# Kernel optimization log

Measured on AMD Instinct MI355X. Metric: run time of the kernel, lower is better.

Reference implementation:

```python
import jax, jax.numpy as jnp
import numpy as np

DIM = 1024
N_HEADS = 16
HEAD_DIM = DIM // N_HEADS
FF_DIM = 4096
EPS = 1e-8


def rms_norm(x, scale):
    # norm = ||x||_2 * d^{-1/2}; out = scale * x / (norm + eps)
    norm = jnp.linalg.norm(x, axis=-1, keepdims=True) * (x.shape[-1] ** -0.5)
    return scale * x / (norm + EPS)


def rope_cos_sin(seq_len, dtype=jnp.float32):
    # inv_freq over even indices of head_dim; after the truncation branch in
    # apply_rotary_pos_emb, effective cos/sin have size head_dim//2.
    inv_freq = 1.0 / (10000.0 ** (jnp.arange(0, HEAD_DIM, 2, dtype=jnp.float32) / HEAD_DIM))
    t = jnp.arange(seq_len, dtype=jnp.float32)
    freqs = t[:, None] * inv_freq[None, :]  # [S, head_dim//2]
    return jnp.cos(freqs).astype(dtype), jnp.sin(freqs).astype(dtype)


def apply_rope(x, cos, sin):
    # x: [B, S, H, hd]; cos/sin: [S, hd//2] broadcast over batch and heads
    c = cos[None, :, None, :]
    s = sin[None, :, None, :]
    x1, x2 = jnp.split(x, 2, axis=-1)
    return jnp.concatenate([x1 * c - x2 * s, x1 * s + x2 * c], axis=-1)


def setup_inputs() -> dict:
    key = jax.random.key(0)
    ks = jax.random.split(key, 10)
    B, S = 2, 2048
    std = DIM ** -0.5
    inp = {
        "x": jax.random.normal(ks[0], (B, S, DIM), jnp.float32),
        "mask": jnp.tril(jnp.ones((S, S), dtype=bool)),
        "qkv_w": jax.random.normal(ks[1], (3 * DIM, DIM), jnp.float32) * std,
        "attn_out_w": jax.random.normal(ks[2], (DIM, DIM), jnp.float32) * std,
        "gate_w": jax.random.normal(ks[3], (FF_DIM, DIM), jnp.float32) * std,
        "gate_b": jnp.zeros((FF_DIM,), jnp.float32),
        "lin_w": jax.random.normal(ks[4], (FF_DIM, DIM), jnp.float32) * std,
        "lin_b": jnp.zeros((FF_DIM,), jnp.float32),
        "ff_out_w": jax.random.normal(ks[5], (DIM, FF_DIM), jnp.float32) * (FF_DIM ** -0.5),
        "norm1_scale": jnp.ones((DIM,), jnp.float32),
        "norm2_scale": jnp.ones((DIM,), jnp.float32),
    }
    return inp


def reference(x, mask, qkv_w, attn_out_w, gate_w, gate_b, lin_w, lin_b,
              ff_out_w, norm1_scale, norm2_scale):
    B, S, _ = x.shape
    residual = x
    qkv = (x @ qkv_w.T).reshape(B, S, 3, N_HEADS, HEAD_DIM)
    q, k, v = qkv[:, :, 0], qkv[:, :, 1], qkv[:, :, 2]  # [B,S,H,hd]
    cos, sin = rope_cos_sin(S, x.dtype)
    q = apply_rope(q, cos, sin)
    k = apply_rope(k, cos, sin)
    # naive full attention, materializing [B,H,S,S] as the source does
    scores = jnp.einsum('bqhd,bkhd->bhqk', q, k) / jnp.sqrt(jnp.asarray(HEAD_DIM, x.dtype))
    scores = jnp.where(mask[None, None, :, :], scores, jnp.asarray(-1e9, x.dtype))
    attn = jax.nn.softmax(scores, axis=-1)
    out = jnp.einsum('bhqk,bkhd->bqhd', attn, v).reshape(B, S, DIM)
    out = out @ attn_out_w.T
    x = rms_norm(residual + out, norm1_scale)
    residual = x
    ff = jax.nn.sigmoid(x @ gate_w.T + gate_b) * (x @ lin_w.T + lin_b)
    ff = ff @ ff_out_w.T
    x = rms_norm(residual + ff, norm2_scale)
    return x
```

## Files before the change

kernel.cpp:

```cpp
#include <hip/hip_runtime.h>
#include <hip/hip_bf16.h>
#include <math.h>

#define DIMSZ 1024
#define NHEAD 16
#define HDIM 64
#define FFDIM 4096
#define SEQ 2048
#define NBATCH 2

typedef unsigned short ushortt;
typedef __attribute__((ext_vector_type(8))) short frag8;
typedef __attribute__((ext_vector_type(4))) float f32x4;

__device__ __forceinline__ float u2f(ushortt u) {
  return __uint_as_float(((unsigned)u) << 16);
}
__device__ __forceinline__ ushortt f2bu(float f) {
  unsigned x = __float_as_uint(f);
  return (ushortt)((x + 0x7FFFu + ((x >> 16) & 1u)) >> 16);
}

__global__ __launch_bounds__(256) void cast_f2b(
    const float* __restrict__ src, ushortt* __restrict__ dst, int n) {
  int i = (blockIdx.x * 256 + threadIdx.x) * 4;
  if (i >= n) return;
  float4 f = *(const float4*)(src + i);
  ushort4 u;
  u.x = f2bu(f.x); u.y = f2bu(f.y); u.z = f2bu(f.z); u.w = f2bu(f.w);
  *(ushort4*)(dst + i) = u;
}

__global__ __launch_bounds__(256) void zero_f32(float* __restrict__ p, int n) {
  int i = (blockIdx.x * 256 + threadIdx.x) * 4;
  if (i < n) *(float4*)(p + i) = make_float4(0.f, 0.f, 0.f, 0.f);
}

template <int EPI, int SK>
__global__ __launch_bounds__(256) void gemm_mfma(
    const ushortt* __restrict__ A, const ushortt* __restrict__ W,
    void* __restrict__ Cv, int M, int N, int K, int KB, size_t skoff) {
  __shared__ __align__(16) short As[2][128 * 32];
  __shared__ __align__(16) short Bs[2][128 * 32];
  const int tid = threadIdx.x;
  const int wave = tid >> 6;
  const int lane = tid & 63;
  int xcd = blockIdx.x & 7, r = blockIdx.x >> 3, kz = 0;
  if (SK == 2) { kz = r & 1; r >>= 1; }
  const int bm = (xcd * 4 + (r & 3)) * 128;
  const int bn = (r >> 2) * 128;
  const int ko0 = kz * KB;
  const int wm = (wave >> 1) * 64;
  const int wn = (wave & 1) * 64;

  f32x4 acc[4][4] = {};

  const int sr = lane >> 2;
  const int sc = (lane & 3) * 8;
  const ushortt* pa0 = A + (size_t)(bm + wave * 16 + sr) * K + ko0 + sc;
  const ushortt* pa1 = pa0 + (size_t)64 * K;
  const ushortt* pb0 = W + (size_t)(bn + wave * 16 + sr) * K + ko0 + sc;
  const ushortt* pb1 = pb0 + (size_t)64 * K;
  const int lo0 = (wave * 16) * 32;
  const int lo1 = (64 + wave * 16) * 32;

  const int fr = lane & 15;
  const int fq = (lane >> 4) * 8;
  const int nt = KB >> 5;

  auto stage = [&](int t, int buf) {
    const int ko = t * 32;
    short* ab = &As[0][0] + buf * 4096;
    short* bb = &Bs[0][0] + buf * 4096;
    __builtin_amdgcn_global_load_lds(
        (const __attribute__((address_space(1))) void*)(pa0 + ko),
        (__attribute__((address_space(3))) void*)(ab + lo0), 16, 0, 0);
    __builtin_amdgcn_global_load_lds(
        (const __attribute__((address_space(1))) void*)(pa1 + ko),
        (__attribute__((address_space(3))) void*)(ab + lo1), 16, 0, 0);
    __builtin_amdgcn_global_load_lds(
        (const __attribute__((address_space(1))) void*)(pb0 + ko),
        (__attribute__((address_space(3))) void*)(bb + lo0), 16, 0, 0);
    __builtin_amdgcn_global_load_lds(
        (const __attribute__((address_space(1))) void*)(pb1 + ko),
        (__attribute__((address_space(3))) void*)(bb + lo1), 16, 0, 0);
  };

  stage(0, 0);
  __syncthreads();

  for (int t = 0; t < nt; ++t) {
    if (t + 1 < nt) stage(t + 1, (t + 1) & 1);
    const short* as = &As[0][0] + (t & 1) * 4096;
    const short* bs = &Bs[0][0] + (t & 1) * 4096;

    frag8 af[4], bf[4];
#pragma unroll
    for (int mi = 0; mi < 4; ++mi)
      af[mi] = *(const frag8*)&as[(wm + mi * 16 + fr) * 32 + fq];
#pragma unroll
    for (int ni = 0; ni < 4; ++ni)
      bf[ni] = *(const frag8*)&bs[(wn + ni * 16 + fr) * 32 + fq];
#pragma unroll
    for (int mi = 0; mi < 4; ++mi)
#pragma unroll
      for (int ni = 0; ni < 4; ++ni)
        acc[mi][ni] = __builtin_amdgcn_mfma_f32_16x16x32_bf16(
            af[mi], bf[ni], acc[mi][ni], 0, 0, 0);
    __syncthreads();
  }

  const int er = (lane >> 4) * 4;
  const int ec = lane & 15;
  float* C0 = (float*)Cv + (SK == 2 ? (size_t)kz * skoff : 0);
#pragma unroll
  for (int mi = 0; mi < 4; ++mi)
#pragma unroll
    for (int ni = 0; ni < 4; ++ni)
#pragma unroll
      for (int r2 = 0; r2 < 4; ++r2) {
        int m = bm + wm + mi * 16 + er + r2;
        int n = bn + wn + ni * 16 + ec;
        size_t o = (size_t)m * N + n;
        float v = acc[mi][ni][r2];
        if (EPI == 0) {
          C0[o] = v;
        } else {
          ((ushortt*)Cv)[o] = f2bu(v);
        }
      }
}

__global__ __launch_bounds__(256) void gemm_gatelin(
    const ushortt* __restrict__ A, const ushortt* __restrict__ Wg,
    const ushortt* __restrict__ Wl, ushortt* __restrict__ Cv,
    const float* __restrict__ gbias, const float* __restrict__ lbias,
    int M, int N, int K) {
  __shared__ __align__(16) short As[2][128 * 32];
  __shared__ __align__(16) short Gs[2][128 * 32];
  __shared__ __align__(16) short Ls[2][128 * 32];
  const int tid = threadIdx.x;
  const int wave = tid >> 6;
  const int lane = tid & 63;
  int xcd = blockIdx.x & 7, r = blockIdx.x >> 3;
  const int bm = (xcd * 4 + (r & 3)) * 128;
  const int bn = (r >> 2) * 128;
  const int wm = (wave >> 1) * 64;
  const int wn = (wave & 1) * 64;

  f32x4 accg[4][4] = {};
  f32x4 accl[4][4] = {};

  const int sr = lane >> 2;
  const int sc = (lane & 3) * 8;
  const ushortt* pa0 = A + (size_t)(bm + wave * 16 + sr) * K + sc;
  const ushortt* pa1 = pa0 + (size_t)64 * K;
  const ushortt* pg0 = Wg + (size_t)(bn + wave * 16 + sr) * K + sc;
  const ushortt* pg1 = pg0 + (size_t)64 * K;
  const ushortt* pl0 = Wl + (size_t)(bn + wave * 16 + sr) * K + sc;
  const ushortt* pl1 = pl0 + (size_t)64 * K;
  const int lo0 = (wave * 16) * 32;
  const int lo1 = (64 + wave * 16) * 32;

  const int fr = lane & 15;
  const int fq = (lane >> 4) * 8;
  const int nt = K >> 5;

  auto stage = [&](int t, int buf) {
    const int ko = t * 32;
    short* ab = &As[0][0] + buf * 4096;
    short* gb = &Gs[0][0] + buf * 4096;
    short* lb = &Ls[0][0] + buf * 4096;
    __builtin_amdgcn_global_load_lds(
        (const __attribute__((address_space(1))) void*)(pa0 + ko),
        (__attribute__((address_space(3))) void*)(ab + lo0), 16, 0, 0);
    __builtin_amdgcn_global_load_lds(
        (const __attribute__((address_space(1))) void*)(pa1 + ko),
        (__attribute__((address_space(3))) void*)(ab + lo1), 16, 0, 0);
    __builtin_amdgcn_global_load_lds(
        (const __attribute__((address_space(1))) void*)(pg0 + ko),
        (__attribute__((address_space(3))) void*)(gb + lo0), 16, 0, 0);
    __builtin_amdgcn_global_load_lds(
        (const __attribute__((address_space(1))) void*)(pg1 + ko),
        (__attribute__((address_space(3))) void*)(gb + lo1), 16, 0, 0);
    __builtin_amdgcn_global_load_lds(
        (const __attribute__((address_space(1))) void*)(pl0 + ko),
        (__attribute__((address_space(3))) void*)(lb + lo0), 16, 0, 0);
    __builtin_amdgcn_global_load_lds(
        (const __attribute__((address_space(1))) void*)(pl1 + ko),
        (__attribute__((address_space(3))) void*)(lb + lo1), 16, 0, 0);
  };

  stage(0, 0);
  __syncthreads();

  for (int t = 0; t < nt; ++t) {
    if (t + 1 < nt) stage(t + 1, (t + 1) & 1);
    const short* as = &As[0][0] + (t & 1) * 4096;
    const short* gs = &Gs[0][0] + (t & 1) * 4096;
    const short* ls = &Ls[0][0] + (t & 1) * 4096;

    frag8 af[4], gf[4], lf[4];
#pragma unroll
    for (int mi = 0; mi < 4; ++mi)
      af[mi] = *(const frag8*)&as[(wm + mi * 16 + fr) * 32 + fq];
#pragma unroll
    for (int ni = 0; ni < 4; ++ni) {
      gf[ni] = *(const frag8*)&gs[(wn + ni * 16 + fr) * 32 + fq];
      lf[ni] = *(const frag8*)&ls[(wn + ni * 16 + fr) * 32 + fq];
    }
#pragma unroll
    for (int mi = 0; mi < 4; ++mi)
#pragma unroll
      for (int ni = 0; ni < 4; ++ni) {
        accg[mi][ni] = __builtin_amdgcn_mfma_f32_16x16x32_bf16(
            af[mi], gf[ni], accg[mi][ni], 0, 0, 0);
        accl[mi][ni] = __builtin_amdgcn_mfma_f32_16x16x32_bf16(
            af[mi], lf[ni], accl[mi][ni], 0, 0, 0);
      }
    __syncthreads();
  }

  const int er = (lane >> 4) * 4;
  const int ec = lane & 15;
#pragma unroll
  for (int mi = 0; mi < 4; ++mi)
#pragma unroll
    for (int ni = 0; ni < 4; ++ni)
#pragma unroll
      for (int r2 = 0; r2 < 4; ++r2) {
        int m = bm + wm + mi * 16 + er + r2;
        int n = bn + wn + ni * 16 + ec;
        size_t o = (size_t)m * N + n;
        float g = accg[mi][ni][r2] + gbias[n];
        float l = accl[mi][ni][r2] + lbias[n];
        float sig = 1.0f / (1.0f + __expf(-g));
        ((ushortt*)Cv)[o] = f2bu(sig * l);
      }
}

__global__ __launch_bounds__(256) void gemm_ffout(
    const ushortt* __restrict__ A, const float* __restrict__ Bw,
    float* __restrict__ C, int koff) {
  __shared__ __align__(16) short As[2][128 * 32];
  __shared__ __align__(16) short Bs[2][128 * 32];
  const int tid = threadIdx.x;
  const int wave = tid >> 6;
  const int lane = tid & 63;
  int xcd = blockIdx.x & 7, r = blockIdx.x >> 3;
  const int kz = r & 1; r >>= 1;
  const int bm = (xcd * 4 + (r & 3)) * 128;
  const int bn = (r >> 2) * 128;
  const int wm = (wave >> 1) * 64;
  const int wn = (wave & 1) * 64;

  f32x4 acc[4][4] = {};

  const int sr = lane >> 2;
  const int sc = (lane & 3) * 8;
  const ushortt* pa0 = A + (size_t)(bm + wave * 16 + sr) * 2048 + kz * 1024 + sc;
  const ushortt* pa1 = pa0 + (size_t)64 * 2048;
  const int lo0 = (wave * 16) * 32;
  const int lo1 = (64 + wave * 16) * 32;

  const int br = tid >> 2;
  const int kc = (tid & 3) * 8;
  const float* pb0 = Bw + (size_t)(bn + br) * FFDIM + koff + kz * 1024 + kc;
  const float* pb1 = pb0 + (size_t)64 * FFDIM;

  const int fr = lane & 15;
  const int fq = (lane >> 4) * 8;
  const int nt = 1024 >> 5;

  float4 f0, f1, f2, f3;
  auto bload = [&](int t) {
    const float* p0 = pb0 + t * 32;
    const float* p1 = pb1 + t * 32;
    f0 = *(const float4*)p0; f1 = *(const float4*)(p0 + 4);
    f2 = *(const float4*)p1; f3 = *(const float4*)(p1 + 4);
  };
  auto pk = [&](float4 a, float4 b) {
    frag8 v;
    v[0] = (short)f2bu(a.x); v[1] = (short)f2bu(a.y);
    v[2] = (short)f2bu(a.z); v[3] = (short)f2bu(a.w);
    v[4] = (short)f2bu(b.x); v[5] = (short)f2bu(b.y);
    v[6] = (short)f2bu(b.z); v[7] = (short)f2bu(b.w);
    return v;
  };
  auto bwrite = [&](int buf) {
    *(frag8*)&Bs[buf][tid * 8] = pk(f0, f1);
    *(frag8*)&Bs[buf][2048 + tid * 8] = pk(f2, f3);
  };
  auto astage = [&](int t, int buf) {
    const int ko = t * 32;
    short* ab = &As[0][0] + buf * 4096;
    __builtin_amdgcn_global_load_lds(
        (const __attribute__((address_space(1))) void*)(pa0 + ko),
        (__attribute__((address_space(3))) void*)(ab + lo0), 16, 0, 0);
    __builtin_amdgcn_global_load_lds(
        (const __attribute__((address_space(1))) void*)(pa1 + ko),
        (__attribute__((address_space(3))) void*)(ab + lo1), 16, 0, 0);
  };

  astage(0, 0);
  bload(0);
  bwrite(0);
  __syncthreads();

  for (int t = 0; t < nt; ++t) {
    if (t + 1 < nt) {
      astage(t + 1, (t + 1) & 1);
      bload(t + 1);
    }
    const short* as = &As[0][0] + (t & 1) * 4096;
    const short* bs = &Bs[0][0] + (t & 1) * 4096;

    frag8 af[4], bf[4];
#pragma unroll
    for (int mi = 0; mi < 4; ++mi)
      af[mi] = *(const frag8*)&as[(wm + mi * 16 + fr) * 32 + fq];
#pragma unroll
    for (int ni = 0; ni < 4; ++ni)
      bf[ni] = *(const frag8*)&bs[(wn + ni * 16 + fr) * 32 + fq];
#pragma unroll
    for (int mi = 0; mi < 4; ++mi)
#pragma unroll
      for (int ni = 0; ni < 4; ++ni)
        acc[mi][ni] = __builtin_amdgcn_mfma_f32_16x16x32_bf16(
            af[mi], bf[ni], acc[mi][ni], 0, 0, 0);
    if (t + 1 < nt) bwrite((t + 1) & 1);
    __syncthreads();
  }

  const int er = (lane >> 4) * 4;
  const int ec = lane & 15;
#pragma unroll
  for (int mi = 0; mi < 4; ++mi)
#pragma unroll
    for (int ni = 0; ni < 4; ++ni)
#pragma unroll
      for (int r2 = 0; r2 < 4; ++r2) {
        int m = bm + wm + mi * 16 + er + r2;
        int n = bn + wn + ni * 16 + ec;
        unsafeAtomicAdd(C + (size_t)m * 1024 + n, acc[mi][ni][r2]);
      }
}

__global__ __launch_bounds__(256) void rope_prep(
    const ushortt* __restrict__ qkv, ushortt* __restrict__ Qr,
    ushortt* __restrict__ Kr, ushortt* __restrict__ Vr) {
  const int s0 = blockIdx.x * 64;
  const int bh = blockIdx.y;
  const int b = bh >> 4, h = bh & 15;
  const int tid = threadIdx.x;
  __shared__ float ifr_s[32];
  __shared__ ushortt vt[64][72];
  if (tid < 32) ifr_s[tid] = __powf(10000.0f, -(float)tid * (1.0f / 32.0f));
  __syncthreads();
  const size_t qbase = (size_t)bh * SEQ * 64;

#pragma unroll
  for (int i = 0; i < 8; ++i) {
    int p = i * 256 + tid;
    int r = p >> 5, d = p & 31;
    size_t src = ((size_t)(b * SEQ + s0 + r)) * (3 * DIMSZ) + h * 64 + d;
    float q1 = u2f(qkv[src]), q2 = u2f(qkv[src + 32]);
    float k1 = u2f(qkv[src + DIMSZ]), k2 = u2f(qkv[src + DIMSZ + 32]);
    float ang = (float)(s0 + r) * ifr_s[d];
    float sn, cs;
    __sincosf(ang, &sn, &cs);
    size_t dst = qbase + (size_t)(s0 + r) * 64 + d;
    Qr[dst]      = f2bu((q1 * cs - q2 * sn) * 0.125f);
    Qr[dst + 32] = f2bu((q1 * sn + q2 * cs) * 0.125f);
    Kr[dst]      = f2bu(k1 * cs - k2 * sn);
    Kr[dst + 32] = f2bu(k1 * sn + k2 * cs);
  }

#pragma unroll
  for (int i = 0; i < 2; ++i) {
    int e = (i * 256 + tid) * 8;
    int r = e >> 6, d0 = e & 63;
    size_t src = ((size_t)(b * SEQ + s0 + r)) * (3 * DIMSZ) + 2 * DIMSZ + h * 64 + d0;
    *(ushort4*)&vt[r][d0]     = *(const ushort4*)(qkv + src);
    *(ushort4*)&vt[r][d0 + 4] = *(const ushort4*)(qkv + src + 4);
  }
  __syncthreads();
  {
    int d = tid >> 2;
    int sc0 = (tid & 3) * 16;
    size_t dst = (size_t)bh * 64 * SEQ + (size_t)blockIdx.x * 4096 +
                 (size_t)d * 64 + sc0;
    ushortt tmp[16];
#pragma unroll
    for (int j = 0; j < 16; ++j) tmp[j] = vt[sc0 + j][d];
    *(ushort4*)(Vr + dst)      = *(ushort4*)&tmp[0];
    *(ushort4*)(Vr + dst + 4)  = *(ushort4*)&tmp[4];
    *(ushort4*)(Vr + dst + 8)  = *(ushort4*)&tmp[8];
    *(ushort4*)(Vr + dst + 12) = *(ushort4*)&tmp[12];
  }
}

__global__ __launch_bounds__(512) void flash_mfma(
    const ushortt* __restrict__ Qr, const ushortt* __restrict__ Kr,
    const ushortt* __restrict__ Vr, ushortt* __restrict__ ctx) {
  const int id = blockIdx.x;
  const int r5 = id & 255;
  const int qt0 = r5 >> 5;
  const int qt = (id & 256) ? (15 - qt0) : qt0;
  const int bh = r5 & 31;
  const int q0 = qt * 128;
  const int b = bh >> 4, h = bh & 15;
  const int tid = threadIdx.x;
  const int w = tid >> 6;
  const int lane = tid & 63;
  const int fr = lane & 15;
  const int quad = lane >> 4;

  __shared__ __align__(16) short Kb[2][4096];
  __shared__ __align__(16) short Vb[2][4096];
  __shared__ __align__(16) ushortt Ps[8][16][72];

  const size_t qkbase = (size_t)bh * SEQ * 64;
  const size_t vbase = (size_t)bh * 64 * SEQ;

  const int lin = (w << 10) + ((lane & 63) << 4);
  const int swz = lin ^ (((lin >> 7) & 7) << 4);
  const char* ksrc = (const char*)(Kr + qkbase) + swz;
  const char* vsrc = (const char*)(Vr + vbase) + swz;
  short* kdst[2] = {&Kb[0][w * 512], &Kb[1][w * 512]};
  short* vdst[2] = {&Vb[0][w * 512], &Vb[1][w * 512]};

  frag8 aq[2];
#pragma unroll
  for (int hh = 0; hh < 2; ++hh)
    aq[hh] = *(const frag8*)(Qr + qkbase + (size_t)(q0 + w * 16 + fr) * 64 +
                             hh * 32 + quad * 8);

  float mr[4], lr[4];
  f32x4 od[4] = {};
#pragma unroll
  for (int r = 0; r < 4; ++r) { mr[r] = -1e30f; lr[r] = 0.0f; }

  const int nt = 2 * qt + 2;

  __builtin_amdgcn_global_load_lds(
      (const __attribute__((address_space(1))) void*)ksrc,
      (__attribute__((address_space(3))) void*)kdst[0], 16, 0, 0);
  __builtin_amdgcn_global_load_lds(
      (const __attribute__((address_space(1))) void*)vsrc,
      (__attribute__((address_space(3))) void*)vdst[0], 16, 0, 0);
  __syncthreads();

  for (int t = 0; t < nt; ++t) {
    const int c0 = t * 64;
    if (t + 1 < nt) {
      const char* kn = ksrc + (size_t)(t + 1) * 8192;
      const char* vn = vsrc + (size_t)(t + 1) * 8192;
      __builtin_amdgcn_global_load_lds(
          (const __attribute__((address_space(1))) void*)kn,
          (__attribute__((address_space(3))) void*)kdst[(t + 1) & 1], 16, 0, 0);
      __builtin_amdgcn_global_load_lds(
          (const __attribute__((address_space(1))) void*)vn,
          (__attribute__((address_space(3))) void*)vdst[(t + 1) & 1], 16, 0, 0);
    }
    const char* kcur = (const char*)Kb[t & 1];
    const char* vcur = (const char*)Vb[t & 1];

    if (c0 <= q0 + w * 16 + 15) {
      f32x4 sc[4] = {};
#pragma unroll
      for (int ni = 0; ni < 4; ++ni)
#pragma unroll
        for (int hh = 0; hh < 2; ++hh) {
          int kb = (((ni * 16 + fr) << 7) + (hh << 6) + (quad << 4)) ^
                   ((fr & 7) << 4);
          frag8 kf = *(const frag8*)(kcur + kb);
          sc[ni] = __builtin_amdgcn_mfma_f32_16x16x32_bf16(aq[hh], kf, sc[ni],
                                                           0, 0, 0);
        }

      if (c0 + 63 > q0 + w * 16) {
        int rowb = q0 + w * 16 + quad * 4;
#pragma unroll
        for (int ni = 0; ni < 4; ++ni) {
          int col = c0 + ni * 16 + fr;
#pragma unroll
          for (int r = 0; r < 4; ++r)
            if (col > rowb + r) sc[ni][r] = -1e30f;
        }
      }

#pragma unroll
      for (int r = 0; r < 4; ++r) {
        float cm = fmaxf(fmaxf(sc[0][r], sc[1][r]), fmaxf(sc[2][r], sc[3][r]));
        for (int off = 1; off < 16; off <<= 1)
          cm = fmaxf(cm, __shfl_xor(cm, off, 16));
        float mn = fmaxf(mr[r], cm);
        float corr = __expf(mr[r] - mn);
        mr[r] = mn;
        float ps = 0.0f;
#pragma unroll
        for (int ni = 0; ni < 4; ++ni) {
          float p = __expf(sc[ni][r] - mn);
          Ps[w][quad * 4 + r][ni * 16 + fr] = f2bu(p);
          ps += p;
        }
        for (int off = 1; off < 16; off <<= 1) ps += __shfl_xor(ps, off, 16);
        lr[r] = lr[r] * corr + ps;
#pragma unroll
        for (int dt = 0; dt < 4; ++dt) od[dt][r] *= corr;
      }

      frag8 pf[2];
#pragma unroll
      for (int hh = 0; hh < 2; ++hh)
        pf[hh] = *(const frag8*)&Ps[w][fr][hh * 32 + quad * 8];
#pragma unroll
      for (int dt = 0; dt < 4; ++dt)
#pragma unroll
        for (int hh = 0; hh < 2; ++hh) {
          int vb_ = (((dt * 16 + fr) << 7) + (hh << 6) + (quad << 4)) ^
                    ((fr & 7) << 4);
          frag8 vf = *(const frag8*)(vcur + vb_);
          od[dt] = __builtin_amdgcn_mfma_f32_16x16x32_bf16(pf[hh], vf, od[dt],
                                                           0, 0, 0);
        }
    }
    __syncthreads();
  }

#pragma unroll
  for (int r = 0; r < 4; ++r) {
    float inv = 1.0f / lr[r];
    size_t row = (size_t)(b * SEQ + q0 + w * 16 + quad * 4 + r) * DIMSZ + h * 64;
#pragma unroll
    for (int dt = 0; dt < 4; ++dt)
      ctx[row + dt * 16 + fr] = f2bu(od[dt][r] * inv);
  }
}

template <int DUAL, int NP>
__global__ __launch_bounds__(256) void add_rmsnorm(
    const float* __restrict__ res, const float* __restrict__ pa,
    const float* __restrict__ pb, const float* __restrict__ scale,
    float* __restrict__ out, ushortt* __restrict__ out2) {
  const int row = blockIdx.x;
  const int tid = threadIdx.x;
  const size_t base = (size_t)row * DIMSZ;
  __shared__ float red[4];
  float y[4];
  float ss = 0.0f;
#pragma unroll
  for (int j = 0; j < 4; ++j) {
    int d = tid + j * 256;
    float yv = res[base + d] + pa[base + d];
    if (NP == 3) yv += pb[base + d];
    y[j] = yv;
    ss += yv * yv;
  }
  for (int off = 1; off < 64; off <<= 1) ss += __shfl_xor(ss, off, 64);
  if ((tid & 63) == 0) red[tid >> 6] = ss;
  __syncthreads();
  float tot = red[0] + red[1] + red[2] + red[3];
  float norm = sqrtf(tot) * 0.03125f;
  float inv = 1.0f / (norm + 1e-8f);
#pragma unroll
  for (int j = 0; j < 4; ++j) {
    int d = tid + j * 256;
    float v = scale[d] * y[j] * inv;
    out[base + d] = v;
    if (DUAL) out2[base + d] = f2bu(v);
  }
}

extern "C" void kernel_launch(void* const* d_in, const int* in_sizes, int n_in,
                              void* d_out, int out_size, void* d_ws, size_t ws_size,
                              hipStream_t stream) {
  const float* x          = (const float*)d_in[0];
  const float* qkv_w      = (const float*)d_in[2];
  const float* attn_out_w = (const float*)d_in[3];
  const float* gate_w     = (const float*)d_in[4];
  const float* gate_b     = (const float*)d_in[5];
  const float* lin_w      = (const float*)d_in[6];
  const float* lin_b      = (const float*)d_in[7];
  const float* ff_out_w   = (const float*)d_in[8];
  const float* n1s        = (const float*)d_in[9];
  const float* n2s        = (const float*)d_in[10];
  float* out = (float*)d_out;

  const int M = NBATCH * SEQ;
  char* ws = (char*)d_ws;
  char* dob = (char*)d_out;
  const size_t MB = 1 << 20;
  ushortt* qkv_tmp = (ushortt*)(ws + 0);
  ushortt* xb      = (ushortt*)(ws + 24 * MB);
  ushortt* qkv_wb  = (ushortt*)(ws + 32 * MB);
  ushortt* Qr      = (ushortt*)(ws + 24 * MB);
  ushortt* Kr      = (ushortt*)(ws + 32 * MB);
  ushortt* Vr      = (ushortt*)(ws + 40 * MB);
  ushortt* attn_wb = (ushortt*)(ws + 24 * MB);
  float*   proj_a  = (float*)(ws + 0);
  float*   proj_b  = (float*)(ws + 40 * MB);
  float*   x1      = (float*)(ws + 16 * MB);
  ushortt* x1b     = (ushortt*)(ws + 32 * MB);
  float*   proj2   = (float*)(ws + 0);
  ushortt* gcb     = (ushortt*)(ws + 40 * MB);
  ushortt* lcb     = (ushortt*)(ws + 44 * MB);
  ushortt* ctx  = (ushortt*)(dob + 0);
  ushortt* ffc  = (ushortt*)(dob + 0);

  cast_f2b<<<4194304 / 1024, 256, 0, stream>>>(x, xb, 4194304);
  cast_f2b<<<3145728 / 1024, 256, 0, stream>>>(qkv_w, qkv_wb, 3145728);
  gemm_mfma<1, 1><<<(3072 / 128) * 32, 256, 0, stream>>>(
      xb, qkv_wb, qkv_tmp, M, 3072, DIMSZ, DIMSZ, 0);
  rope_prep<<<dim3(SEQ / 64, NBATCH * NHEAD), 256, 0, stream>>>(
      qkv_tmp, Qr, Kr, Vr);
  flash_mfma<<<(SEQ / 128) * NBATCH * NHEAD, 512, 0, stream>>>(
      Qr, Kr, Vr, ctx);
  cast_f2b<<<1048576 / 1024, 256, 0, stream>>>(attn_out_w, attn_wb, 1048576);
  gemm_mfma<0, 2><<<(DIMSZ / 128) * 32 * 2, 256, 0, stream>>>(
      ctx, attn_wb, proj_a, M, DIMSZ, DIMSZ, 512,
      (size_t)(40 * MB) / sizeof(float));
  add_rmsnorm<1, 3><<<M, 256, 0, stream>>>(x, proj_a, proj_b, n1s, x1, x1b);
  zero_f32<<<4194304 / 1024, 256, 0, stream>>>(proj2, 4194304);
  for (int c = 0; c < 2; ++c) {
    cast_f2b<<<2048, 256, 0, stream>>>(
        gate_w + (size_t)c * 2097152, gcb, 2097152);
    cast_f2b<<<2048, 256, 0, stream>>>(
        lin_w + (size_t)c * 2097152, lcb, 2097152);
    gemm_gatelin<<<(2048 / 128) * 32, 256, 0, stream>>>(
        x1b, gcb, lcb, ffc, gate_b + c * 2048, lin_b + c * 2048,
        M, 2048, DIMSZ);
    gemm_ffout<<<(1024 / 128) * 32 * 2, 256, 0, stream>>>(
        ffc, ff_out_w, proj2, c * 2048);
  }
  add_rmsnorm<0, 2><<<M, 256, 0, stream>>>(x1, proj2, nullptr, n2s, out,
                                           nullptr);
}
```

Measured before the change: 563.9 us.

## Replace syncthreads with partial vmcnt waits to overlap prefetch with compute

In the GEMM, fused gate GEMM, atomic split-K GEMM and flash attention loops, the full __syncthreads (which drains all outstanding global loads) is replaced by explicit s_waitcnt vmcnt(N), raw s_barrier and sched_barrier. Only the loads for the current tile are waited on, so next-tile prefetch stays in flight while MFMAs run. The code now depends on exact in-flight load counts per thread, and a wrong count could read LDS before it is filled. sched_barrier also stops the compiler from moving instructions across these points.

```diff
diff --git a/kernel.cpp b/kernel.cpp
--- a/kernel.cpp
+++ b/kernel.cpp
@@ -87,10 +87,16 @@
   };
 
   stage(0, 0);
-  __syncthreads();
 
   for (int t = 0; t < nt; ++t) {
-    if (t + 1 < nt) stage(t + 1, (t + 1) & 1);
+    if (t + 1 < nt) {
+      stage(t + 1, (t + 1) & 1);
+      asm volatile("s_waitcnt vmcnt(4)" ::: "memory");
+    } else {
+      asm volatile("s_waitcnt vmcnt(0)" ::: "memory");
+    }
+    __builtin_amdgcn_s_barrier();
+    __builtin_amdgcn_sched_barrier(0);
     const short* as = &As[0][0] + (t & 1) * 4096;
     const short* bs = &Bs[0][0] + (t & 1) * 4096;
 
@@ -107,7 +113,8 @@
       for (int ni = 0; ni < 4; ++ni)
         acc[mi][ni] = __builtin_amdgcn_mfma_f32_16x16x32_bf16(
             af[mi], bf[ni], acc[mi][ni], 0, 0, 0);
-    __syncthreads();
+    __builtin_amdgcn_sched_barrier(0);
+    __builtin_amdgcn_s_barrier();
   }
 
   const int er = (lane >> 4) * 4;
@@ -192,10 +199,16 @@
   };
 
   stage(0, 0);
-  __syncthreads();
 
   for (int t = 0; t < nt; ++t) {
-    if (t + 1 < nt) stage(t + 1, (t + 1) & 1);
+    if (t + 1 < nt) {
+      stage(t + 1, (t + 1) & 1);
+      asm volatile("s_waitcnt vmcnt(6)" ::: "memory");
+    } else {
+      asm volatile("s_waitcnt vmcnt(0)" ::: "memory");
+    }
+    __builtin_amdgcn_s_barrier();
+    __builtin_amdgcn_sched_barrier(0);
     const short* as = &As[0][0] + (t & 1) * 4096;
     const short* gs = &Gs[0][0] + (t & 1) * 4096;
     const short* ls = &Ls[0][0] + (t & 1) * 4096;
@@ -218,7 +231,8 @@
         accl[mi][ni] = __builtin_amdgcn_mfma_f32_16x16x32_bf16(
             af[mi], lf[ni], accl[mi][ni], 0, 0, 0);
       }
-    __syncthreads();
+    __builtin_amdgcn_sched_barrier(0);
+    __builtin_amdgcn_s_barrier();
   }
 
   const int er = (lane >> 4) * 4;
@@ -302,16 +316,21 @@
         (__attribute__((address_space(3))) void*)(ab + lo1), 16, 0, 0);
   };
 
+  bload(0);
   astage(0, 0);
-  bload(0);
   bwrite(0);
-  __syncthreads();
+  asm volatile("s_waitcnt lgkmcnt(0)" ::: "memory");
 
   for (int t = 0; t < nt; ++t) {
     if (t + 1 < nt) {
+      bload(t + 1);
       astage(t + 1, (t + 1) & 1);
-      bload(t + 1);
+      asm volatile("s_waitcnt vmcnt(6)" ::: "memory");
+    } else {
+      asm volatile("s_waitcnt vmcnt(0)" ::: "memory");
     }
+    __builtin_amdgcn_s_barrier();
+    __builtin_amdgcn_sched_barrier(0);
     const short* as = &As[0][0] + (t & 1) * 4096;
     const short* bs = &Bs[0][0] + (t & 1) * 4096;
 
@@ -329,7 +348,9 @@
         acc[mi][ni] = __builtin_amdgcn_mfma_f32_16x16x32_bf16(
             af[mi], bf[ni], acc[mi][ni], 0, 0, 0);
     if (t + 1 < nt) bwrite((t + 1) & 1);
-    __syncthreads();
+    asm volatile("s_waitcnt lgkmcnt(0)" ::: "memory");
+    __builtin_amdgcn_sched_barrier(0);
+    __builtin_amdgcn_s_barrier();
   }
 
   const int er = (lane >> 4) * 4;
@@ -449,7 +470,6 @@
   __builtin_amdgcn_global_load_lds(
       (const __attribute__((address_space(1))) void*)vsrc,
       (__attribute__((address_space(3))) void*)vdst[0], 16, 0, 0);
-  __syncthreads();
 
   for (int t = 0; t < nt; ++t) {
     const int c0 = t * 64;
@@ -462,7 +482,12 @@
       __builtin_amdgcn_global_load_lds(
           (const __attribute__((address_space(1))) void*)vn,
           (__attribute__((address_space(3))) void*)vdst[(t + 1) & 1], 16, 0, 0);
+      asm volatile("s_waitcnt vmcnt(2)" ::: "memory");
+    } else {
+      asm volatile("s_waitcnt vmcnt(0)" ::: "memory");
     }
+    __builtin_amdgcn_s_barrier();
+    __builtin_amdgcn_sched_barrier(0);
     const char* kcur = (const char*)Kb[t & 1];
     const char* vcur = (const char*)Vb[t & 1];
 
@@ -526,7 +551,8 @@
                                                            0, 0, 0);
         }
     }
-    __syncthreads();
+    __builtin_amdgcn_sched_barrier(0);
+    __builtin_amdgcn_s_barrier();
   }
 
 #pragma unroll
```

Result: no change. 558.0 us (-1.1%).
